# Performance work log

Measured on AMD Instinct MI355X. Metric: run time of the kernel, lower is better.

## Reference

```python
import jax, jax.numpy as jnp
import numpy as np

IGNORE_INDEX = -100
BETA = 0.1
B2, T, H, V = 8, 512, 2048, 32000  # B2 = 2*B (chosen + rejected concatenated)


def setup_inputs() -> dict:
    key = jax.random.key(0)
    k1, k2, k3, k4, k5 = jax.random.split(key, 5)
    bound = 1.0 / np.sqrt(H)  # torch.nn.Linear default init
    x = jax.random.normal(k1, (B2, T, H), dtype=jnp.float32)
    ref_x = jax.random.normal(k2, (B2, T, H), dtype=jnp.float32)
    y = jax.random.randint(k3, (B2, T), 0, V, dtype=jnp.int64)
    W = jax.random.uniform(k4, (V, H), dtype=jnp.float32, minval=-bound, maxval=bound)
    ref_W = jax.random.uniform(k5, (V, H), dtype=jnp.float32, minval=-bound, maxval=bound)
    return {"x": x, "ref_x": ref_x, "y": y, "W": W, "ref_W": ref_W}


def _avg_logps(h, w, y):
    # fused linear + log-softmax + label gather, averaged over valid tokens
    logits = jnp.einsum('bth,vh->btv', h, w)          # [B2, T, V]
    lsm = jax.nn.log_softmax(logits, axis=-1)
    mask = y != IGNORE_INDEX                          # [B2, T]
    y_safe = jnp.where(mask, y, 0)
    tok_logps = jnp.take_along_axis(lsm, y_safe[..., None], axis=-1)[..., 0]
    tok_logps = jnp.where(mask, tok_logps, 0.0)
    n_valid = jnp.maximum(mask.sum(axis=-1), 1)
    return tok_logps.sum(axis=-1) / n_valid           # [B2] average log-prob per sequence


def reference(x, ref_x, y, W, ref_W):
    pol_logps = _avg_logps(x, W, y)
    # reference model runs under no_grad in Liger
    ref_logps = jax.lax.stop_gradient(_avg_logps(ref_x, ref_W, y))
    B = x.shape[0] // 2
    chosen, rejected = pol_logps[:B], pol_logps[B:]
    ref_chosen, ref_rejected = ref_logps[:B], ref_logps[B:]
    logits_diff = BETA * ((chosen - ref_chosen) - (rejected - ref_rejected))
    loss = -jax.nn.log_sigmoid(logits_diff).sum() / B
    return loss
```

## Files before the change

### kernel.cpp

```cpp
#include <hip/hip_runtime.h>
#include <hip/hip_bf16.h>
#include <stdint.h>

#define K_DIM 2048
#define NTOK  4096
#define VOCAB 32000
#define BETA  0.1f

typedef __attribute__((ext_vector_type(8))) short short8;
typedef __attribute__((ext_vector_type(8))) int   int8v;
typedef __attribute__((ext_vector_type(4))) float f32x4;

union frag8 { int8v v; struct { int4 lo, hi; } s; };

__device__ __forceinline__ unsigned short f2bf(float f) {
  unsigned u = __float_as_uint(f);
  u += 0x7FFFu + ((u >> 16) & 1u);
  return (unsigned short)(u >> 16);
}

__device__ __forceinline__ void gload_lds16(const void* g, void* l) {
  __builtin_amdgcn_global_load_lds(
      (const __attribute__((address_space(1))) void*)g,
      (__attribute__((address_space(3))) void*)l, 16, 0, 0);
}

__global__ void cvt_all_fp8(const float* __restrict__ x, const float* __restrict__ rx,
                            const float* __restrict__ W, const float* __restrict__ rW,
                            unsigned char* __restrict__ Xb, unsigned char* __restrict__ rXb,
                            unsigned char* __restrict__ Wb, unsigned char* __restrict__ rWb) {
  const int which = blockIdx.y;
  const float* in;
  unsigned char* out;
  int n8;
  if (which == 0)      { in = x;  out = Xb;  n8 = NTOK * K_DIM / 8; }
  else if (which == 1) { in = rx; out = rXb; n8 = NTOK * K_DIM / 8; }
  else if (which == 2) { in = W;  out = Wb;  n8 = VOCAB * K_DIM / 8; }
  else                 { in = rW; out = rWb; n8 = VOCAB * K_DIM / 8; }
  int i = blockIdx.x * blockDim.x + threadIdx.x;
  int stride = gridDim.x * blockDim.x;
  for (; i < n8; i += stride) {
    float4 a = ((const float4*)in)[2 * i];
    float4 b = ((const float4*)in)[2 * i + 1];
    int lo = __builtin_amdgcn_cvt_pk_fp8_f32(a.x, a.y, 0, false);
    lo     = __builtin_amdgcn_cvt_pk_fp8_f32(a.z, a.w, lo, true);
    int hi = __builtin_amdgcn_cvt_pk_fp8_f32(b.x, b.y, 0, false);
    hi     = __builtin_amdgcn_cvt_pk_fp8_f32(b.z, b.w, hi, true);
    ((int2*)out)[i] = make_int2(lo, hi);
  }
}

__global__ __launch_bounds__(256)
void gemm_lse_fp8(const unsigned char* __restrict__ A0, const unsigned char* __restrict__ A1,
                  const unsigned char* __restrict__ B0, const unsigned char* __restrict__ B1,
                  float* __restrict__ sumexp) {
  __shared__ unsigned char smA[128 * 128];
  __shared__ unsigned char smB[128 * 128];
  const int tid  = threadIdx.x;
  const int lane = tid & 63;
  const int wid  = tid >> 6;
  const int wm = wid & 1, wn = wid >> 1;
  const int m0 = blockIdx.x * 128;
  const int n0 = blockIdx.y * 128;
  const int model = blockIdx.z;
  const unsigned char* Ag = model ? A1 : A0;
  const unsigned char* Bg = model ? B1 : B0;

  f32x4 acc[4][4];
#pragma unroll
  for (int i = 0; i < 4; i++)
#pragma unroll
    for (int j = 0; j < 4; j++) acc[i][j] = (f32x4){0.f, 0.f, 0.f, 0.f};

  const int rowin = lane >> 3;
  const int kb    = ((lane & 7) ^ rowin) * 16;
  const int quad  = lane >> 4;
  const int l15   = lane & 15;
  const int l7    = lane & 7;

  for (int k0 = 0; k0 < K_DIM; k0 += 128) {
#pragma unroll
    for (int c = wid; c < 16; c += 4) {
      gload_lds16(Ag + (size_t)(m0 + c * 8 + rowin) * K_DIM + k0 + kb, &smA[c * 1024]);
      gload_lds16(Bg + (size_t)(n0 + c * 8 + rowin) * K_DIM + k0 + kb, &smB[c * 1024]);
    }
    __syncthreads();
    const int p0 = ((quad * 2)     ^ l7) * 16;
    const int p1 = ((quad * 2 + 1) ^ l7) * 16;
    frag8 af[4], bf[4];
#pragma unroll
    for (int i = 0; i < 4; i++) {
      const unsigned char* r = &smA[(wm * 64 + i * 16 + l15) * 128];
      af[i].s.lo = *(const int4*)(r + p0);
      af[i].s.hi = *(const int4*)(r + p1);
    }
#pragma unroll
    for (int j = 0; j < 4; j++) {
      const unsigned char* r = &smB[(wn * 64 + j * 16 + l15) * 128];
      bf[j].s.lo = *(const int4*)(r + p0);
      bf[j].s.hi = *(const int4*)(r + p1);
    }
#pragma unroll
    for (int i = 0; i < 4; i++)
#pragma unroll
      for (int j = 0; j < 4; j++)
        acc[i][j] = __builtin_amdgcn_mfma_scale_f32_16x16x128_f8f6f4(
            af[i].v, bf[j].v, acc[i][j], 0, 0, 0, 127, 0, 127);
    __syncthreads();
  }

  float rs[4][4];
#pragma unroll
  for (int i = 0; i < 4; i++)
#pragma unroll
    for (int r = 0; r < 4; r++) rs[i][r] = 0.f;
#pragma unroll
  for (int i = 0; i < 4; i++)
#pragma unroll
    for (int j = 0; j < 4; j++)
#pragma unroll
      for (int r = 0; r < 4; r++) rs[i][r] += __expf(acc[i][j][r]);
#pragma unroll
  for (int i = 0; i < 4; i++)
#pragma unroll
    for (int r = 0; r < 4; r++) {
      float v = rs[i][r];
      v += __shfl_xor(v, 1, 64);
      v += __shfl_xor(v, 2, 64);
      v += __shfl_xor(v, 4, 64);
      v += __shfl_xor(v, 8, 64);
      rs[i][r] = v;
    }
  if ((lane & 15) == 0) {
#pragma unroll
    for (int i = 0; i < 4; i++)
#pragma unroll
      for (int r = 0; r < 4; r++) {
        int row = m0 + wm * 64 + i * 16 + quad * 4 + r;
        atomicAdd(&sumexp[model * NTOK + row], rs[i][r]);
      }
  }
}

__global__ __launch_bounds__(256)
void gemm_lse_f32(const float* __restrict__ A0, const float* __restrict__ A1,
                  const float* __restrict__ B0, const float* __restrict__ B1,
                  float* __restrict__ sumexp) {
  __shared__ unsigned short smA[128 * 64];
  __shared__ unsigned short smB[128 * 64];
  const int tid  = threadIdx.x;
  const int lane = tid & 63;
  const int wid  = tid >> 6;
  const int wm = wid & 1, wn = wid >> 1;
  const int m0 = blockIdx.x * 128;
  const int n0 = blockIdx.y * 128;
  const int model = blockIdx.z;
  const float* Agf = model ? A1 : A0;
  const float* Bgf = model ? B1 : B0;

  f32x4 acc[4][4];
#pragma unroll
  for (int i = 0; i < 4; i++)
#pragma unroll
    for (int j = 0; j < 4; j++) acc[i][j] = (f32x4){0.f, 0.f, 0.f, 0.f};

  for (int k0 = 0; k0 < K_DIM; k0 += 64) {
#pragma unroll
    for (int i = 0; i < 8; i++) {
      int f = tid + i * 256;
      int row = f >> 4, kc = (f & 15) * 4;
      int pos = (((kc >> 3) ^ (row & 7)) << 3) + (kc & 7);
      float4 va = *(const float4*)(Agf + (size_t)(m0 + row) * K_DIM + k0 + kc);
      float4 vb = *(const float4*)(Bgf + (size_t)(n0 + row) * K_DIM + k0 + kc);
      ushort4 ha, hb;
      ha.x = f2bf(va.x); ha.y = f2bf(va.y); ha.z = f2bf(va.z); ha.w = f2bf(va.w);
      hb.x = f2bf(vb.x); hb.y = f2bf(vb.y); hb.z = f2bf(vb.z); hb.w = f2bf(vb.w);
      *(ushort4*)&smA[row * 64 + pos] = ha;
      *(ushort4*)&smB[row * 64 + pos] = hb;
    }
    __syncthreads();
    const int quad = lane >> 4;
    const int l7   = lane & 7;
#pragma unroll
    for (int s = 0; s < 2; s++) {
      short8 af[4], bf[4];
      const int cpos = ((s * 4 + quad) ^ l7) * 8;
#pragma unroll
      for (int i = 0; i < 4; i++)
        af[i] = *(const short8*)&smA[(wm * 64 + i * 16 + (lane & 15)) * 64 + cpos];
#pragma unroll
      for (int j = 0; j < 4; j++)
        bf[j] = *(const short8*)&smB[(wn * 64 + j * 16 + (lane & 15)) * 64 + cpos];
#pragma unroll
      for (int i = 0; i < 4; i++)
#pragma unroll
        for (int j = 0; j < 4; j++)
          acc[i][j] = __builtin_amdgcn_mfma_f32_16x16x32_bf16(af[i], bf[j], acc[i][j], 0, 0, 0);
    }
    __syncthreads();
  }

  float rs[4][4];
#pragma unroll
  for (int i = 0; i < 4; i++)
#pragma unroll
    for (int r = 0; r < 4; r++) rs[i][r] = 0.f;
#pragma unroll
  for (int i = 0; i < 4; i++)
#pragma unroll
    for (int j = 0; j < 4; j++)
#pragma unroll
      for (int r = 0; r < 4; r++) rs[i][r] += __expf(acc[i][j][r]);
#pragma unroll
  for (int i = 0; i < 4; i++)
#pragma unroll
    for (int r = 0; r < 4; r++) {
      float v = rs[i][r];
      v += __shfl_xor(v, 1, 64);
      v += __shfl_xor(v, 2, 64);
      v += __shfl_xor(v, 4, 64);
      v += __shfl_xor(v, 8, 64);
      rs[i][r] = v;
    }
  if ((lane & 15) == 0) {
    int quad = lane >> 4;
#pragma unroll
    for (int i = 0; i < 4; i++)
#pragma unroll
      for (int r = 0; r < 4; r++) {
        int row = m0 + wm * 64 + i * 16 + quad * 4 + r;
        atomicAdd(&sumexp[model * NTOK + row], rs[i][r]);
      }
  }
}

__global__ void tgt_kernel(const float* __restrict__ x, const float* __restrict__ rx,
                           const float* __restrict__ W, const float* __restrict__ rW,
                           const int* __restrict__ y, float* __restrict__ tgt) {
  int g = blockIdx.x * blockDim.x + threadIdx.x;
  int gw = g >> 6;
  int lane = g & 63;
  int model = gw >> 12;
  int token = gw & (NTOK - 1);
  int yi = y[token];
  float s = 0.f;
  if (yi >= 0) {
    const float* xv = (model ? rx : x) + (size_t)token * K_DIM;
    const float* wv = (model ? rW : W) + (size_t)yi * K_DIM;
#pragma unroll
    for (int i = 0; i < 8; i++) {
      int p = (lane + i * 64) * 4;
      float4 a = *(const float4*)(xv + p);
      float4 b = *(const float4*)(wv + p);
      s += a.x * b.x + a.y * b.y + a.z * b.z + a.w * b.w;
    }
  }
  for (int off = 32; off; off >>= 1) s += __shfl_xor(s, off, 64);
  if (lane == 0) tgt[gw] = s;
}

__global__ void finalize(const float* __restrict__ sumexp, const float* __restrict__ tgt,
                         const int* __restrict__ y, float* __restrict__ out) {
  __shared__ float ssum[16];
  __shared__ int scnt[8];
  if (threadIdx.x < 16) ssum[threadIdx.x] = 0.f;
  if (threadIdx.x < 8) scnt[threadIdx.x] = 0;
  __syncthreads();
  for (int idx = threadIdx.x; idx < 2 * NTOK; idx += blockDim.x) {
    int model = idx >> 12;
    int token = idx & (NTOK - 1);
    int row = token >> 9;
    int yi = y[token];
    if (yi != -100) {
      float v = tgt[idx] - logf(sumexp[idx]);
      atomicAdd(&ssum[model * 8 + row], v);
      if (model == 0) atomicAdd(&scnt[row], 1);
    }
  }
  __syncthreads();
  if (threadIdx.x == 0) {
    float lp[16];
    for (int m = 0; m < 2; m++)
      for (int r = 0; r < 8; r++) {
        int n = scnt[r] > 0 ? scnt[r] : 1;
        lp[m * 8 + r] = ssum[m * 8 + r] / (float)n;
      }
    float loss = 0.f;
    for (int b = 0; b < 4; b++) {
      float z = BETA * ((lp[b] - lp[8 + b]) - (lp[b + 4] - lp[12 + b]));
      float l = (z > 0.f) ? log1pf(expf(-z)) : (-z + log1pf(expf(z)));
      loss += l;
    }
    out[0] = loss / 4.f;
  }
}

extern "C" void kernel_launch(void* const* d_in, const int* in_sizes, int n_in,
                              void* d_out, int out_size, void* d_ws, size_t ws_size,
                              hipStream_t stream) {
  const float* x  = (const float*)d_in[0];
  const float* rx = (const float*)d_in[1];
  const int*   y  = (const int*)d_in[2];
  const float* W  = (const float*)d_in[3];
  const float* rW = (const float*)d_in[4];
  float* out = (float*)d_out;

  char* ws = (char*)d_ws;
  float* sumexp = (float*)ws;
  float* tgt    = (float*)(ws + 32 * 1024);
  hipMemsetAsync(d_ws, 0, 64 * 1024, stream);

  const size_t XB_ELEMS = (size_t)NTOK * K_DIM;
  const size_t WB_ELEMS = (size_t)VOCAB * K_DIM;
  const size_t NEED = 64 * 1024 + 2 * (XB_ELEMS + WB_ELEMS);

  dim3 ggrid(NTOK / 128, VOCAB / 128, 2);

  if (ws_size >= NEED) {
    unsigned char* Xb  = (unsigned char*)(ws + 64 * 1024);
    unsigned char* rXb = Xb + XB_ELEMS;
    unsigned char* Wb  = rXb + XB_ELEMS;
    unsigned char* rWb = Wb + WB_ELEMS;
    cvt_all_fp8<<<dim3(8192, 4), 256, 0, stream>>>(x, rx, W, rW, Xb, rXb, Wb, rWb);
    gemm_lse_fp8<<<ggrid, 256, 0, stream>>>(Xb, rXb, Wb, rWb, sumexp);
  } else {
    gemm_lse_f32<<<ggrid, 256, 0, stream>>>(x, rx, W, rW, sumexp);
  }

  tgt_kernel<<<2048, 256, 0, stream>>>(x, rx, W, rW, y, tgt);
  finalize<<<1, 256, 0, stream>>>(sumexp, tgt, y, out);
}
```

Before: 1.306 ms.

## Triple-buffer FP8 GEMM tiles with 512-thread blocks and XCD-aware tile remap

Rewrites the FP8 GEMM+logsumexp kernel to use 256x128 tiles computed by 8 waves, with a three-stage LDS ring buffer filled by async global-to-LDS loads and explicit vmcnt waits. Loads for future K-steps now overlap the MFMA work of the current one, instead of loading and computing in strict sequence. A swizzled 1D grid maps consecutive blocks across XCDs so that blocks sharing a tile run on the same XCD, which should improve L2 reuse. The price is 144KB of LDS per block, so only one block fits per CU, and the hand-written waitcnt counts must match the number of loads issued.

```diff
diff --git a/kernel.cpp b/kernel.cpp
--- a/kernel.cpp
+++ b/kernel.cpp
@@ -23,6 +23,12 @@
   __builtin_amdgcn_global_load_lds(
       (const __attribute__((address_space(1))) void*)g,
       (__attribute__((address_space(3))) void*)l, 16, 0, 0);
+}
+
+template<int N> __device__ __forceinline__ void vwait() {
+  if constexpr (N == 12)      asm volatile("s_waitcnt vmcnt(12)" ::: "memory");
+  else if constexpr (N == 6)  asm volatile("s_waitcnt vmcnt(6)"  ::: "memory");
+  else if constexpr (N == 0)  asm volatile("s_waitcnt vmcnt(0)"  ::: "memory");
 }
 
 __global__ void cvt_all_fp8(const float* __restrict__ x, const float* __restrict__ rx,
@@ -50,21 +56,31 @@
   }
 }
 
-__global__ __launch_bounds__(256)
+__global__ __launch_bounds__(512, 1)
 void gemm_lse_fp8(const unsigned char* __restrict__ A0, const unsigned char* __restrict__ A1,
                   const unsigned char* __restrict__ B0, const unsigned char* __restrict__ B1,
                   float* __restrict__ sumexp) {
-  __shared__ unsigned char smA[128 * 128];
-  __shared__ unsigned char smB[128 * 128];
+  __shared__ unsigned char sm[3 * 49152];
   const int tid  = threadIdx.x;
   const int lane = tid & 63;
   const int wid  = tid >> 6;
-  const int wm = wid & 1, wn = wid >> 1;
-  const int m0 = blockIdx.x * 128;
-  const int n0 = blockIdx.y * 128;
+  const int wm   = wid >> 1;
+  const int wn   = wid & 1;
+
+  const int d  = blockIdx.x;
+  const int w  = (d & 7) * 500 + (d >> 3);
+  const int m0 = (w & 15) * 256;
+  const int n0 = (w >> 4) * 128;
   const int model = blockIdx.z;
-  const unsigned char* Ag = model ? A1 : A0;
-  const unsigned char* Bg = model ? B1 : B0;
+  const unsigned char* __restrict__ Ag = model ? A1 : A0;
+  const unsigned char* __restrict__ Bg = model ? B1 : B0;
+
+  unsigned char* sA0 = sm;
+  unsigned char* sB0 = sm + 32768;
+  unsigned char* sA1 = sm + 49152;
+  unsigned char* sB1 = sm + 49152 + 32768;
+  unsigned char* sA2 = sm + 98304;
+  unsigned char* sB2 = sm + 98304 + 32768;
 
   f32x4 acc[4][4];
 #pragma unroll
@@ -72,42 +88,72 @@
 #pragma unroll
     for (int j = 0; j < 4; j++) acc[i][j] = (f32x4){0.f, 0.f, 0.f, 0.f};
 
-  const int rowin = lane >> 3;
-  const int kb    = ((lane & 7) ^ rowin) * 16;
-  const int quad  = lane >> 4;
-  const int l15   = lane & 15;
-  const int l7    = lane & 7;
-
-  for (int k0 = 0; k0 < K_DIM; k0 += 128) {
-#pragma unroll
-    for (int c = wid; c < 16; c += 4) {
-      gload_lds16(Ag + (size_t)(m0 + c * 8 + rowin) * K_DIM + k0 + kb, &smA[c * 1024]);
-      gload_lds16(Bg + (size_t)(n0 + c * 8 + rowin) * K_DIM + k0 + kb, &smB[c * 1024]);
-    }
-    __syncthreads();
-    const int p0 = ((quad * 2)     ^ l7) * 16;
-    const int p1 = ((quad * 2 + 1) ^ l7) * 16;
-    frag8 af[4], bf[4];
-#pragma unroll
-    for (int i = 0; i < 4; i++) {
-      const unsigned char* r = &smA[(wm * 64 + i * 16 + l15) * 128];
-      af[i].s.lo = *(const int4*)(r + p0);
-      af[i].s.hi = *(const int4*)(r + p1);
-    }
-#pragma unroll
-    for (int j = 0; j < 4; j++) {
-      const unsigned char* r = &smB[(wn * 64 + j * 16 + l15) * 128];
-      bf[j].s.lo = *(const int4*)(r + p0);
-      bf[j].s.hi = *(const int4*)(r + p1);
-    }
-#pragma unroll
-    for (int i = 0; i < 4; i++)
-#pragma unroll
-      for (int j = 0; j < 4; j++)
-        acc[i][j] = __builtin_amdgcn_mfma_scale_f32_16x16x128_f8f6f4(
-            af[i].v, bf[j].v, acc[i][j], 0, 0, 0, 127, 0, 127);
-    __syncthreads();
-  }
+  const int rsub = lane >> 3;
+  const int jsw  = ((lane & 7) ^ rsub) * 16;
+  const int q    = lane >> 4;
+  const int l15  = lane & 15, l7 = lane & 7;
+  const int p0   = ((2 * q)     ^ l7) * 16;
+  const int p1   = ((2 * q + 1) ^ l7) * 16;
+
+  auto stage = [&](int k0, unsigned char* bufA, unsigned char* bufB) {
+#pragma unroll
+    for (int c = 0; c < 4; ++c) {
+      int cc = c * 8 + wid;
+      gload_lds16(Ag + (size_t)(m0 + cc * 8 + rsub) * K_DIM + k0 + jsw, bufA + cc * 1024);
+    }
+#pragma unroll
+    for (int c = 0; c < 2; ++c) {
+      int cc = c * 8 + wid;
+      gload_lds16(Bg + (size_t)(n0 + cc * 8 + rsub) * K_DIM + k0 + jsw, bufB + cc * 1024);
+    }
+  };
+
+#define GBODY(T, SA, SB, DOSTAGE, VMN, HASNEXT)                               \
+  do {                                                                        \
+    frag8 af[4], bf[4];                                                       \
+    _Pragma("unroll") for (int i = 0; i < 4; i++) {                           \
+      const unsigned char* rp = SA + (wm * 64 + i * 16 + l15) * 128;          \
+      af[i].s.lo = *(const int4*)(rp + p0);                                   \
+      af[i].s.hi = *(const int4*)(rp + p1);                                   \
+    }                                                                         \
+    _Pragma("unroll") for (int j = 0; j < 4; j++) {                           \
+      const unsigned char* rp = SB + (wn * 64 + j * 16 + l15) * 128;          \
+      bf[j].s.lo = *(const int4*)(rp + p0);                                   \
+      bf[j].s.hi = *(const int4*)(rp + p1);                                   \
+    }                                                                         \
+    __builtin_amdgcn_s_setprio(1);                                            \
+    _Pragma("unroll") for (int i = 0; i < 4; i++)                             \
+      _Pragma("unroll") for (int j = 0; j < 4; j++)                           \
+        acc[i][j] = __builtin_amdgcn_mfma_scale_f32_16x16x128_f8f6f4(         \
+            af[i].v, bf[j].v, acc[i][j], 0, 0, 0, 127, 0, 127);               \
+    __builtin_amdgcn_s_setprio(0);                                            \
+    if (HASNEXT) {                                                            \
+      asm volatile("s_waitcnt lgkmcnt(0)" ::: "memory");   \
+      vwait<VMN>();                       \
+      __builtin_amdgcn_sched_barrier(0);         \
+      __builtin_amdgcn_s_barrier();                                           \
+      if (DOSTAGE) stage((T + 3) * 128, SA, SB);     \
+    }                                                                         \
+  } while (0)
+
+  stage(0,   sA0, sB0);
+  stage(128, sA1, sB1);
+  stage(256, sA2, sB2);
+  vwait<12>();
+  __builtin_amdgcn_sched_barrier(0);
+  __builtin_amdgcn_s_barrier();
+
+#pragma unroll
+  for (int tb = 0; tb < 12; tb += 3) {
+    GBODY(tb,     sA0, sB0, 1, 6, 1);
+    GBODY(tb + 1, sA1, sB1, 1, 6, 1);
+    GBODY(tb + 2, sA2, sB2, 1, 6, 1);
+  }
+  GBODY(12, sA0, sB0, 1, 6, 1);
+  GBODY(13, sA1, sB1, 0, 6, 1);
+  GBODY(14, sA2, sB2, 0, 0, 1);
+  GBODY(15, sA0, sB0, 0, -1, 0);
+#undef GBODY
 
   float rs[4][4];
 #pragma unroll
@@ -136,7 +182,7 @@
     for (int i = 0; i < 4; i++)
 #pragma unroll
       for (int r = 0; r < 4; r++) {
-        int row = m0 + wm * 64 + i * 16 + quad * 4 + r;
+        int row = m0 + wm * 64 + i * 16 + q * 4 + r;
         atomicAdd(&sumexp[model * NTOK + row], rs[i][r]);
       }
   }
@@ -314,17 +360,15 @@
   const size_t WB_ELEMS = (size_t)VOCAB * K_DIM;
   const size_t NEED = 64 * 1024 + 2 * (XB_ELEMS + WB_ELEMS);
 
-  dim3 ggrid(NTOK / 128, VOCAB / 128, 2);
-
   if (ws_size >= NEED) {
     unsigned char* Xb  = (unsigned char*)(ws + 64 * 1024);
     unsigned char* rXb = Xb + XB_ELEMS;
     unsigned char* Wb  = rXb + XB_ELEMS;
     unsigned char* rWb = Wb + WB_ELEMS;
     cvt_all_fp8<<<dim3(8192, 4), 256, 0, stream>>>(x, rx, W, rW, Xb, rXb, Wb, rWb);
-    gemm_lse_fp8<<<ggrid, 256, 0, stream>>>(Xb, rXb, Wb, rWb, sumexp);
+    gemm_lse_fp8<<<dim3(4000, 1, 2), 512, 0, stream>>>(Xb, rXb, Wb, rWb, sumexp);
   } else {
-    gemm_lse_f32<<<ggrid, 256, 0, stream>>>(x, rx, W, rW, sumexp);
+    gemm_lse_f32<<<dim3(32, 250, 2), 256, 0, stream>>>(x, rx, W, rW, sumexp);
   }
 
   tgt_kernel<<<2048, 256, 0, stream>>>(x, rx, W, rW, y, tgt);
```

Result: slower. 1.427 ms (+9.3%).
